# Kernel optimization log

Hardware: AMD Instinct MI355X
Metric: run time of the kernel (lower is better)

The kernel has to match this reference:

```python
import jax, jax.numpy as jnp
import numpy as np

IGNORE_INDEX = 255
KEEP_RATIO = 0.3
MIN_KEPT = 100000
LABEL_SMOOTHING = 0.0


def setup_inputs() -> dict:
    key = jax.random.key(0)
    k1, k2 = jax.random.split(key)
    logits = jax.random.normal(k1, (8, 19, 512, 1024), dtype=jnp.float32)
    labels = jax.random.randint(k2, (8, 512, 1024), 0, 19, dtype=jnp.int64)
    return {"logits": logits, "labels": labels}


def reference(logits, labels):
    B, C, H, W = logits.shape
    # per-pixel cross entropy (reduction='none'), flattened to [N]
    logp = jax.nn.log_softmax(logits, axis=1)                      # [B,C,H,W]
    logp_flat = logp.transpose(0, 2, 3, 1).reshape(-1, C)          # [N,C]
    lab = labels.reshape(-1)                                       # [N]
    valid = lab != IGNORE_INDEX
    safe_lab = jnp.where(valid, lab, 0)
    nll = -jnp.take_along_axis(logp_flat, safe_lab[:, None], axis=1)[:, 0]
    smooth = -jnp.mean(logp_flat, axis=1)
    loss = (1.0 - LABEL_SMOOTHING) * nll + LABEL_SMOOTHING * smooth
    # torch CE with ignore_index gives 0 loss at ignored pixels
    loss = jnp.where(valid, loss, 0.0)

    n_valid = jnp.sum(valid).astype(jnp.int32)
    n_keep = jnp.maximum((KEEP_RATIO * n_valid.astype(jnp.float32)).astype(jnp.int32),
                         jnp.minimum(MIN_KEPT, n_valid))
    n_keep = jnp.minimum(n_keep, n_valid)

    # sort valid losses descending; invalid pixels pushed to the end via -inf
    masked = jnp.where(valid, loss, -jnp.inf)
    sorted_desc = -jnp.sort(-masked)
    thr = jax.lax.stop_gradient(sorted_desc[jnp.maximum(n_keep - 1, 0)])
    thr = jnp.where(n_keep < n_valid, thr, -jnp.inf)

    keep = valid & (masked >= thr)
    cnt = jnp.sum(keep).astype(loss.dtype)
    total = jnp.sum(jnp.where(keep, loss, 0.0))
    mean_kept = total / jnp.maximum(cnt, 1.0)
    # n_valid == 0 -> 0.0 (matches logits.sum()*0.0)
    return jnp.where(n_valid == 0, jnp.sum(logits) * 0.0, mean_kept)
```

## Files before the change

kernel.cpp:

```cpp
#include <hip/hip_runtime.h>
#include <math.h>

#define IGN 255
constexpr int NC = 19;
constexpr int HWsz = 512 * 1024;
constexpr int NPIX = 8 * HWsz;

typedef float v4f __attribute__((ext_vector_type(4)));
typedef int v4i __attribute__((ext_vector_type(4)));
typedef unsigned v4u __attribute__((ext_vector_type(4)));

struct Ctl {
  double total;
  unsigned n_valid, cnt, done, pad;
};

constexpr size_t H0 = 256;
constexpr size_t H1 = H0 + 2048 * 4;
constexpr size_t H2 = H1 + 2048 * 4;
constexpr size_t LOSS_OFF = 65536;

__device__ inline unsigned flip_key(unsigned u) {
  unsigned mask = (unsigned)((int)u >> 31) | 0x80000000u;
  return u ^ mask;
}
__device__ inline float unflip_val(unsigned k) {
  unsigned u = (k & 0x80000000u) ? (k ^ 0x80000000u) : ~k;
  return __uint_as_float(u);
}
__device__ inline unsigned compute_k(unsigned nv) {
  int nk = (int)(0.3f * (float)nv);
  int mk = (100000 < (int)nv) ? 100000 : (int)nv;
  if (nk < mk) nk = mk;
  if (nk > (int)nv) nk = (int)nv;
  return (unsigned)nk;
}

template <int NB>
__device__ inline void selscan(const unsigned* __restrict__ hist, unsigned k,
                               unsigned& bin, unsigned& kk) {
  constexpr int BPT = NB / 256;
  __shared__ unsigned ts[256];
  __shared__ unsigned bb[2];
  int t = threadIdx.x;
  unsigned local[BPT];
  unsigned lsum = 0;
#pragma unroll
  for (int j = 0; j < BPT; ++j) { local[j] = hist[t * BPT + j]; lsum += local[j]; }
  ts[t] = lsum;
  __syncthreads();
  for (int off = 1; off < 256; off <<= 1) {
    unsigned add = (t + off < 256) ? ts[t + off] : 0u;
    __syncthreads();
    ts[t] += add;
    __syncthreads();
  }
  unsigned above = ts[t] - lsum;
  if (t == 0) { bb[0] = 0xFFFFFFFFu; bb[1] = 0u; }
  __syncthreads();
  if (k > 0) {
#pragma unroll
    for (int j = BPT - 1; j >= 0; --j) {
      unsigned cb = local[j];
      unsigned tot = above + cb;
      if (above < k && tot >= k) { bb[0] = (unsigned)(t * BPT + j); bb[1] = k - above; }
      above = tot;
    }
  }
  __syncthreads();
  bin = bb[0];
  kk = bb[1];
  __syncthreads();
}

__global__ void k_init(unsigned char* ws) {
  Ctl* ctl = (Ctl*)ws;
  unsigned* h = (unsigned*)(ws + H0);
  int t = threadIdx.x;
  if (t == 0) { ctl->total = 0.0; ctl->n_valid = 0; ctl->cnt = 0; ctl->done = 0; }
  for (int i = t; i < 5120; i += 256) h[i] = 0;
}

__global__ __launch_bounds__(256) void k_loss(const float* __restrict__ logits,
                                              const int* __restrict__ labels,
                                              unsigned char* __restrict__ ws) {
  Ctl* ctl = (Ctl*)ws;
  float* loss = (float*)(ws + LOSS_OFF);
  unsigned* h0 = (unsigned*)(ws + H0);
  __shared__ unsigned lh[2048];
  __shared__ unsigned red[256];
  for (int i = threadIdx.x; i < 2048; i += 256) lh[i] = 0;
  __syncthreads();

  int t = threadIdx.x;
  int base = blockIdx.x * 4096;
  int b = base >> 19;
  int hw = base & (HWsz - 1);
  const float* lbase = logits + (size_t)(b * NC) * HWsz + hw + t * 4;

  v4i labv[4];
#pragma unroll
  for (int q = 0; q < 4; ++q)
    labv[q] = *reinterpret_cast<const v4i*>(labels + base + q * 1024 + t * 4);

  v4f m[4], s[4], vl[4];
#pragma unroll
  for (int q = 0; q < 4; ++q) {
    v4f v = *reinterpret_cast<const v4f*>(lbase + q * 1024);
    m[q] = v;
    s[q] = (v4f)(1.f);
#pragma unroll
    for (int j = 0; j < 4; ++j)
      vl[q][j] = (labv[q][j] == 0) ? v[j] : 0.f;
  }

#pragma unroll 1
  for (int c = 1; c < NC; ++c) {
    const float* cb = lbase + (size_t)c * HWsz;
    v4f v[4];
#pragma unroll
    for (int q = 0; q < 4; ++q)
      v[q] = *reinterpret_cast<const v4f*>(cb + q * 1024);
#pragma unroll
    for (int q = 0; q < 4; ++q) {
#pragma unroll
      for (int j = 0; j < 4; ++j) {
        float x = v[q][j];
        float mo = m[q][j];
        float mn = fmaxf(mo, x);
        s[q][j] = s[q][j] * __expf(mo - mn) + __expf(x - mn);
        m[q][j] = mn;
        vl[q][j] = (labv[q][j] == c) ? x : vl[q][j];
      }
    }
  }

  unsigned cnt = 0;
#pragma unroll
  for (int q = 0; q < 4; ++q) {
    v4f o;
#pragma unroll
    for (int j = 0; j < 4; ++j) {
      int lb = labv[q][j];
      float lse = m[q][j] + __logf(s[q][j]);
      o[j] = (lb == IGN) ? -INFINITY : (lse - vl[q][j]);
      cnt += (lb != IGN);
      atomicAdd(&lh[flip_key(__float_as_uint(o[j])) >> 21], 1u);
    }
    *reinterpret_cast<v4f*>(loss + base + q * 1024 + t * 4) = o;
  }

  red[t] = cnt;
  __syncthreads();
  for (int s2 = 128; s2 > 0; s2 >>= 1) {
    if (t < s2) red[t] += red[t + s2];
    __syncthreads();
  }
  if (t == 0 && red[0]) atomicAdd(&ctl->n_valid, red[0]);
  for (int i = t; i < 2048; i += 256)
    if (lh[i]) atomicAdd(&h0[i], lh[i]);
}

__global__ __launch_bounds__(256) void k_hist1(unsigned char* __restrict__ ws) {
  Ctl* ctl = (Ctl*)ws;
  const unsigned* keys = (const unsigned*)(ws + LOSS_OFF);
  unsigned* h0 = (unsigned*)(ws + H0);
  unsigned* h1 = (unsigned*)(ws + H1);
  __shared__ unsigned lh[2048];
  unsigned k0 = compute_k(ctl->n_valid);
  unsigned p0, k1;
  selscan<2048>(h0, k0, p0, k1);
  for (int i = threadIdx.x; i < 2048; i += 256) lh[i] = 0;
  __syncthreads();

  unsigned idx0 = blockIdx.x * 512 + threadIdx.x;
#pragma unroll
  for (int i = 0; i < 2; ++i) {
    v4u u = reinterpret_cast<const v4u*>(keys)[idx0 + i * 256];
#pragma unroll
    for (int j = 0; j < 4; ++j) {
      unsigned key = flip_key(u[j]);
      if ((key >> 21) == p0) atomicAdd(&lh[(key >> 10) & 0x7FFu], 1u);
    }
  }
  __syncthreads();
  for (int i = threadIdx.x; i < 2048; i += 256)
    if (lh[i]) atomicAdd(&h1[i], lh[i]);
}

__global__ __launch_bounds__(256) void k_hist2(unsigned char* __restrict__ ws) {
  Ctl* ctl = (Ctl*)ws;
  const unsigned* keys = (const unsigned*)(ws + LOSS_OFF);
  unsigned* h0 = (unsigned*)(ws + H0);
  unsigned* h1 = (unsigned*)(ws + H1);
  unsigned* h2 = (unsigned*)(ws + H2);
  __shared__ unsigned lh[1024];
  unsigned k0 = compute_k(ctl->n_valid);
  unsigned p0, k1, p1, k2;
  selscan<2048>(h0, k0, p0, k1);
  selscan<2048>(h1, k1, p1, k2);
  unsigned pp = (p0 << 11) | p1;
  for (int i = threadIdx.x; i < 1024; i += 256) lh[i] = 0;
  __syncthreads();

  unsigned idx0 = blockIdx.x * 512 + threadIdx.x;
#pragma unroll
  for (int i = 0; i < 2; ++i) {
    v4u u = reinterpret_cast<const v4u*>(keys)[idx0 + i * 256];
#pragma unroll
    for (int j = 0; j < 4; ++j) {
      unsigned key = flip_key(u[j]);
      if ((key >> 10) == pp) atomicAdd(&lh[key & 0x3FFu], 1u);
    }
  }
  __syncthreads();
  for (int i = threadIdx.x; i < 1024; i += 256)
    if (lh[i]) atomicAdd(&h2[i], lh[i]);
}

__global__ __launch_bounds__(256) void k_final(unsigned char* __restrict__ ws,
                                               float* __restrict__ out) {
  Ctl* ctl = (Ctl*)ws;
  const float* loss = (const float*)(ws + LOSS_OFF);
  unsigned* h0 = (unsigned*)(ws + H0);
  unsigned* h1 = (unsigned*)(ws + H1);
  unsigned* h2 = (unsigned*)(ws + H2);
  unsigned k0 = compute_k(ctl->n_valid);
  unsigned p0, k1, p1, k2, b2, kf;
  selscan<2048>(h0, k0, p0, k1);
  selscan<2048>(h1, k1, p1, k2);
  selscan<1024>(h2, k2, b2, kf);
  float thr = INFINITY;
  if (k0 > 0) thr = unflip_val((((p0 << 11) | p1) << 10) | b2);

  unsigned idx0 = blockIdx.x * 512 + threadIdx.x;
  float s = 0.f;
  unsigned c = 0;
#pragma unroll
  for (int i = 0; i < 2; ++i) {
    v4f v = reinterpret_cast<const v4f*>(loss)[idx0 + i * 256];
    if (v[0] >= thr) { s += v[0]; c++; }
    if (v[1] >= thr) { s += v[1]; c++; }
    if (v[2] >= thr) { s += v[2]; c++; }
    if (v[3] >= thr) { s += v[3]; c++; }
  }
  double sd = (double)s;
  for (int off = 32; off > 0; off >>= 1) {
    sd += __shfl_down(sd, off);
    c += __shfl_down(c, off);
  }
  __shared__ double sred[4];
  __shared__ unsigned cred[4];
  int wave = threadIdx.x >> 6, lane = threadIdx.x & 63;
  if (lane == 0) { sred[wave] = sd; cred[wave] = c; }
  __syncthreads();
  if (threadIdx.x == 0) {
    double st = sred[0] + sred[1] + sred[2] + sred[3];
    unsigned ct = cred[0] + cred[1] + cred[2] + cred[3];
    atomicAdd(&ctl->total, st);
    atomicAdd(&ctl->cnt, ct);
    __threadfence();
    unsigned prev = atomicAdd(&ctl->done, 1u);
    if (prev == gridDim.x - 1) {
      double tt = atomicAdd(&ctl->total, 0.0);
      unsigned cc = atomicAdd(&ctl->cnt, 0u);
      float r = 0.f;
      if (ctl->n_valid != 0) {
        if (cc < 1u) cc = 1u;
        r = (float)(tt / (double)cc);
      }
      out[0] = r;
    }
  }
}

extern "C" void kernel_launch(void* const* d_in, const int* in_sizes, int n_in,
                              void* d_out, int out_size, void* d_ws, size_t ws_size,
                              hipStream_t stream) {
  const float* logits = (const float*)d_in[0];
  const int* labels = (const int*)d_in[1];
  float* out = (float*)d_out;
  unsigned char* ws = (unsigned char*)d_ws;

  hipLaunchKernelGGL(k_init, dim3(1), dim3(256), 0, stream, ws);
  hipLaunchKernelGGL(k_loss, dim3(NPIX / 4096), dim3(256), 0, stream, logits, labels, ws);
  hipLaunchKernelGGL(k_hist1, dim3(NPIX / 8 / 256), dim3(256), 0, stream, ws);
  hipLaunchKernelGGL(k_hist2, dim3(NPIX / 8 / 256), dim3(256), 0, stream, ws);
  hipLaunchKernelGGL(k_final, dim3(NPIX / 8 / 256), dim3(256), 0, stream, ws, out);
}
```

Measured before the change: 206.0 us.

## Drop max-tracking softmax, prefetch logits, fold kept-sum into radix passes

The loss kernel now computes log-sum-exp as a plain sum of exp without a running max, packs labels into bytes, and software-prefetches channel planes two ahead with nontemporal loads. Per-wave shared histograms reduce atomic contention. The radix-select passes accumulate the sum and count of elements strictly above the current prefix, plus a per-bin sum for the last level. This removes the separate full scan in the final kernel and leaves a single-block epilogue. Dropping the max subtraction risks overflow for large logits, and float atomic per-bin sums may change rounding.

```diff
diff --git a/kernel.cpp b/kernel.cpp
--- a/kernel.cpp
+++ b/kernel.cpp
@@ -1,7 +1,7 @@
 #include <hip/hip_runtime.h>
 #include <math.h>
 
-#define IGN 255
+#define IGN 255u
 constexpr int NC = 19;
 constexpr int HWsz = 512 * 1024;
 constexpr int NPIX = 8 * HWsz;
@@ -11,14 +11,18 @@
 typedef unsigned v4u __attribute__((ext_vector_type(4)));
 
 struct Ctl {
-  double total;
-  unsigned n_valid, cnt, done, pad;
+  double s_above;
+  unsigned long long c_above;
+  unsigned n_valid;
+  unsigned pad;
 };
 
 constexpr size_t H0 = 256;
-constexpr size_t H1 = H0 + 2048 * 4;
-constexpr size_t H2 = H1 + 2048 * 4;
-constexpr size_t LOSS_OFF = 65536;
+constexpr size_t H1 = H0 + 8192;
+constexpr size_t H2 = H1 + 8192;
+constexpr size_t SUM2 = H2 + 4096;
+constexpr size_t KEYS = 65536;
+constexpr size_t ZERO_BYTES = SUM2 + 4096;
 
 __device__ inline unsigned flip_key(unsigned u) {
   unsigned mask = (unsigned)((int)u >> 31) | 0x80000000u;
@@ -73,81 +77,75 @@
   __syncthreads();
 }
 
-__global__ void k_init(unsigned char* ws) {
-  Ctl* ctl = (Ctl*)ws;
-  unsigned* h = (unsigned*)(ws + H0);
-  int t = threadIdx.x;
-  if (t == 0) { ctl->total = 0.0; ctl->n_valid = 0; ctl->cnt = 0; ctl->done = 0; }
-  for (int i = t; i < 5120; i += 256) h[i] = 0;
-}
-
 __global__ __launch_bounds__(256) void k_loss(const float* __restrict__ logits,
                                               const int* __restrict__ labels,
                                               unsigned char* __restrict__ ws) {
   Ctl* ctl = (Ctl*)ws;
-  float* loss = (float*)(ws + LOSS_OFF);
   unsigned* h0 = (unsigned*)(ws + H0);
-  __shared__ unsigned lh[2048];
+  unsigned* keys = (unsigned*)(ws + KEYS);
+  __shared__ unsigned lh[4 * 2048];
   __shared__ unsigned red[256];
-  for (int i = threadIdx.x; i < 2048; i += 256) lh[i] = 0;
-  __syncthreads();
-
-  int t = threadIdx.x;
-  int base = blockIdx.x * 4096;
+  int t = threadIdx.x;
+  for (int i = t; i < 8192; i += 256) lh[i] = 0;
+  __syncthreads();
+
+  int base = blockIdx.x * 2048;
   int b = base >> 19;
   int hw = base & (HWsz - 1);
-  const float* lbase = logits + (size_t)(b * NC) * HWsz + hw + t * 4;
-
-  v4i labv[4];
-#pragma unroll
-  for (int q = 0; q < 4; ++q)
-    labv[q] = *reinterpret_cast<const v4i*>(labels + base + q * 1024 + t * 4);
-
-  v4f m[4], s[4], vl[4];
-#pragma unroll
-  for (int q = 0; q < 4; ++q) {
-    v4f v = *reinterpret_cast<const v4f*>(lbase + q * 1024);
-    m[q] = v;
-    s[q] = (v4f)(1.f);
-#pragma unroll
-    for (int j = 0; j < 4; ++j)
-      vl[q][j] = (labv[q][j] == 0) ? v[j] : 0.f;
-  }
+  const float* lp = logits + (size_t)(b * NC) * HWsz + hw + t * 4;
+
+  unsigned labp[2];
+#pragma unroll
+  for (int q = 0; q < 2; ++q) {
+    v4i l = *reinterpret_cast<const v4i*>(labels + base + q * 1024 + t * 4);
+    labp[q] = (unsigned)(l[0] & 255) | ((unsigned)(l[1] & 255) << 8) |
+              ((unsigned)(l[2] & 255) << 16) | ((unsigned)(l[3] & 255) << 24);
+  }
+
+  v4f s[2] = {(v4f)(0.f), (v4f)(0.f)};
+  v4f vl[2] = {(v4f)(0.f), (v4f)(0.f)};
+  v4f cur[2], nxt[2];
+  cur[0] = __builtin_nontemporal_load(reinterpret_cast<const v4f*>(lp));
+  cur[1] = __builtin_nontemporal_load(reinterpret_cast<const v4f*>(lp + 1024));
+  nxt[0] = __builtin_nontemporal_load(reinterpret_cast<const v4f*>(lp + HWsz));
+  nxt[1] = __builtin_nontemporal_load(reinterpret_cast<const v4f*>(lp + HWsz + 1024));
 
 #pragma unroll 1
-  for (int c = 1; c < NC; ++c) {
-    const float* cb = lbase + (size_t)c * HWsz;
-    v4f v[4];
-#pragma unroll
-    for (int q = 0; q < 4; ++q)
-      v[q] = *reinterpret_cast<const v4f*>(cb + q * 1024);
-#pragma unroll
-    for (int q = 0; q < 4; ++q) {
+  for (int c = 0; c < NC; ++c) {
+    v4f fut0 = cur[0], fut1 = cur[1];
+    if (c + 2 < NC) {
+      const float* fp = lp + (size_t)(c + 2) * HWsz;
+      fut0 = __builtin_nontemporal_load(reinterpret_cast<const v4f*>(fp));
+      fut1 = __builtin_nontemporal_load(reinterpret_cast<const v4f*>(fp + 1024));
+    }
+    unsigned cc = (unsigned)c;
+#pragma unroll
+    for (int q = 0; q < 2; ++q) {
 #pragma unroll
       for (int j = 0; j < 4; ++j) {
-        float x = v[q][j];
-        float mo = m[q][j];
-        float mn = fmaxf(mo, x);
-        s[q][j] = s[q][j] * __expf(mo - mn) + __expf(x - mn);
-        m[q][j] = mn;
-        vl[q][j] = (labv[q][j] == c) ? x : vl[q][j];
+        float x = cur[q][j];
+        s[q][j] += __expf(x);
+        vl[q][j] = (((labp[q] >> (8 * j)) & 255u) == cc) ? x : vl[q][j];
       }
     }
+    cur[0] = nxt[0]; cur[1] = nxt[1];
+    nxt[0] = fut0;  nxt[1] = fut1;
   }
 
   unsigned cnt = 0;
-#pragma unroll
-  for (int q = 0; q < 4; ++q) {
-    v4f o;
+  unsigned lw = (unsigned)(t >> 6) * 2048u;
+#pragma unroll
+  for (int q = 0; q < 2; ++q) {
+    v4u kv;
 #pragma unroll
     for (int j = 0; j < 4; ++j) {
-      int lb = labv[q][j];
-      float lse = m[q][j] + __logf(s[q][j]);
-      o[j] = (lb == IGN) ? -INFINITY : (lse - vl[q][j]);
+      unsigned lb = (labp[q] >> (8 * j)) & 255u;
+      float o = (lb == IGN) ? -INFINITY : (__logf(s[q][j]) - vl[q][j]);
+      kv[j] = flip_key(__float_as_uint(o));
       cnt += (lb != IGN);
-      atomicAdd(&lh[flip_key(__float_as_uint(o[j])) >> 21], 1u);
-    }
-    *reinterpret_cast<v4f*>(loss + base + q * 1024 + t * 4) = o;
+      atomicAdd(&lh[lw + (kv[j] >> 21)], 1u);
+    }
+    *reinterpret_cast<v4u*>(keys + base + q * 1024 + t * 4) = kv;
   }
 
   red[t] = cnt;
@@ -157,120 +155,157 @@
     __syncthreads();
   }
   if (t == 0 && red[0]) atomicAdd(&ctl->n_valid, red[0]);
-  for (int i = t; i < 2048; i += 256)
-    if (lh[i]) atomicAdd(&h0[i], lh[i]);
-}
-
-__global__ __launch_bounds__(256) void k_hist1(unsigned char* __restrict__ ws) {
+  for (int i = t; i < 2048; i += 256) {
+    unsigned v = lh[i] + lh[2048 + i] + lh[4096 + i] + lh[6144 + i];
+    if (v) atomicAdd(&h0[i], v);
+  }
+}
+
+__global__ __launch_bounds__(256) void k_pass1(unsigned char* __restrict__ ws) {
   Ctl* ctl = (Ctl*)ws;
-  const unsigned* keys = (const unsigned*)(ws + LOSS_OFF);
-  unsigned* h0 = (unsigned*)(ws + H0);
+  const unsigned* keys = (const unsigned*)(ws + KEYS);
+  const unsigned* h0 = (const unsigned*)(ws + H0);
   unsigned* h1 = (unsigned*)(ws + H1);
   __shared__ unsigned lh[2048];
+  int t = threadIdx.x;
   unsigned k0 = compute_k(ctl->n_valid);
   unsigned p0, k1;
   selscan<2048>(h0, k0, p0, k1);
-  for (int i = threadIdx.x; i < 2048; i += 256) lh[i] = 0;
-  __syncthreads();
-
-  unsigned idx0 = blockIdx.x * 512 + threadIdx.x;
-#pragma unroll
-  for (int i = 0; i < 2; ++i) {
-    v4u u = reinterpret_cast<const v4u*>(keys)[idx0 + i * 256];
+  for (int i = t; i < 2048; i += 256) lh[i] = 0;
+  __syncthreads();
+
+  int base = blockIdx.x * 2048 + t * 4;
+  float fs = 0.f;
+  unsigned fc = 0;
+#pragma unroll
+  for (int q = 0; q < 2; ++q) {
+    v4u kv = *reinterpret_cast<const v4u*>(keys + base + q * 1024);
 #pragma unroll
     for (int j = 0; j < 4; ++j) {
-      unsigned key = flip_key(u[j]);
-      if ((key >> 21) == p0) atomicAdd(&lh[(key >> 10) & 0x7FFu], 1u);
-    }
-  }
-  __syncthreads();
-  for (int i = threadIdx.x; i < 2048; i += 256)
+      unsigned key = kv[j];
+      unsigned pre = key >> 21;
+      if (pre > p0) { fs += unflip_val(key); fc++; }
+      else if (pre == p0) atomicAdd(&lh[(key >> 10) & 0x7FFu], 1u);
+    }
+  }
+  __syncthreads();
+  for (int i = t; i < 2048; i += 256)
     if (lh[i]) atomicAdd(&h1[i], lh[i]);
-}
-
-__global__ __launch_bounds__(256) void k_hist2(unsigned char* __restrict__ ws) {
+
+  double sd = (double)fs;
+  for (int off = 32; off > 0; off >>= 1) {
+    sd += __shfl_down(sd, off);
+    fc += __shfl_down(fc, off);
+  }
+  __shared__ double sred[4];
+  __shared__ unsigned cred[4];
+  int wave = t >> 6, lane = t & 63;
+  if (lane == 0) { sred[wave] = sd; cred[wave] = fc; }
+  __syncthreads();
+  if (t == 0) {
+    double st = sred[0] + sred[1] + sred[2] + sred[3];
+    unsigned long long ct = (unsigned long long)(cred[0] + cred[1] + cred[2] + cred[3]);
+    if (st != 0.0) atomicAdd(&ctl->s_above, st);
+    if (ct) atomicAdd(&ctl->c_above, ct);
+  }
+}
+
+__global__ __launch_bounds__(256) void k_pass2(unsigned char* __restrict__ ws) {
   Ctl* ctl = (Ctl*)ws;
-  const unsigned* keys = (const unsigned*)(ws + LOSS_OFF);
-  unsigned* h0 = (unsigned*)(ws + H0);
-  unsigned* h1 = (unsigned*)(ws + H1);
+  const unsigned* keys = (const unsigned*)(ws + KEYS);
+  const unsigned* h0 = (const unsigned*)(ws + H0);
+  const unsigned* h1 = (const unsigned*)(ws + H1);
   unsigned* h2 = (unsigned*)(ws + H2);
+  float* sum2 = (float*)(ws + SUM2);
   __shared__ unsigned lh[1024];
+  int t = threadIdx.x;
   unsigned k0 = compute_k(ctl->n_valid);
   unsigned p0, k1, p1, k2;
   selscan<2048>(h0, k0, p0, k1);
   selscan<2048>(h1, k1, p1, k2);
-  unsigned pp = (p0 << 11) | p1;
-  for (int i = threadIdx.x; i < 1024; i += 256) lh[i] = 0;
-  __syncthreads();
-
-  unsigned idx0 = blockIdx.x * 512 + threadIdx.x;
-#pragma unroll
-  for (int i = 0; i < 2; ++i) {
-    v4u u = reinterpret_cast<const v4u*>(keys)[idx0 + i * 256];
+  for (int i = t; i < 1024; i += 256) lh[i] = 0;
+  __syncthreads();
+
+  int base = blockIdx.x * 2048 + t * 4;
+  float fs = 0.f;
+  unsigned fc = 0;
+#pragma unroll
+  for (int q = 0; q < 2; ++q) {
+    v4u kv = *reinterpret_cast<const v4u*>(keys + base + q * 1024);
 #pragma unroll
     for (int j = 0; j < 4; ++j) {
-      unsigned key = flip_key(u[j]);
-      if ((key >> 10) == pp) atomicAdd(&lh[key & 0x3FFu], 1u);
-    }
-  }
-  __syncthreads();
-  for (int i = threadIdx.x; i < 1024; i += 256)
+      unsigned key = kv[j];
+      if ((key >> 21) == p0) {
+        unsigned mid = (key >> 10) & 0x7FFu;
+        if (mid > p1) { fs += unflip_val(key); fc++; }
+        else if (mid == p1) {
+          atomicAdd(&lh[key & 0x3FFu], 1u);
+          atomicAdd(&sum2[key & 0x3FFu], unflip_val(key));
+        }
+      }
+    }
+  }
+  __syncthreads();
+  for (int i = t; i < 1024; i += 256)
     if (lh[i]) atomicAdd(&h2[i], lh[i]);
-}
-
-__global__ __launch_bounds__(256) void k_final(unsigned char* __restrict__ ws,
-                                               float* __restrict__ out) {
+
+  double sd = (double)fs;
+  for (int off = 32; off > 0; off >>= 1) {
+    sd += __shfl_down(sd, off);
+    fc += __shfl_down(fc, off);
+  }
+  __shared__ double sred[4];
+  __shared__ unsigned cred[4];
+  int wave = t >> 6, lane = t & 63;
+  if (lane == 0) { sred[wave] = sd; cred[wave] = fc; }
+  __syncthreads();
+  if (t == 0) {
+    double st = sred[0] + sred[1] + sred[2] + sred[3];
+    unsigned long long ct = (unsigned long long)(cred[0] + cred[1] + cred[2] + cred[3]);
+    if (st != 0.0) atomicAdd(&ctl->s_above, st);
+    if (ct) atomicAdd(&ctl->c_above, ct);
+  }
+}
+
+__global__ __launch_bounds__(256) void k_epi(unsigned char* __restrict__ ws,
+                                             float* __restrict__ out) {
   Ctl* ctl = (Ctl*)ws;
-  const float* loss = (const float*)(ws + LOSS_OFF);
-  unsigned* h0 = (unsigned*)(ws + H0);
-  unsigned* h1 = (unsigned*)(ws + H1);
-  unsigned* h2 = (unsigned*)(ws + H2);
-  unsigned k0 = compute_k(ctl->n_valid);
+  const unsigned* h0 = (const unsigned*)(ws + H0);
+  const unsigned* h1 = (const unsigned*)(ws + H1);
+  const unsigned* h2 = (const unsigned*)(ws + H2);
+  const float* sum2 = (const float*)(ws + SUM2);
+  int t = threadIdx.x;
+  unsigned nv = ctl->n_valid;
+  unsigned k0 = compute_k(nv);
   unsigned p0, k1, p1, k2, b2, kf;
   selscan<2048>(h0, k0, p0, k1);
   selscan<2048>(h1, k1, p1, k2);
   selscan<1024>(h2, k2, b2, kf);
-  float thr = INFINITY;
-  if (k0 > 0) thr = unflip_val((((p0 << 11) | p1) << 10) | b2);
-
-  unsigned idx0 = blockIdx.x * 512 + threadIdx.x;
-  float s = 0.f;
-  unsigned c = 0;
-#pragma unroll
-  for (int i = 0; i < 2; ++i) {
-    v4f v = reinterpret_cast<const v4f*>(loss)[idx0 + i * 256];
-    if (v[0] >= thr) { s += v[0]; c++; }
-    if (v[1] >= thr) { s += v[1]; c++; }
-    if (v[2] >= thr) { s += v[2]; c++; }
-    if (v[3] >= thr) { s += v[3]; c++; }
-  }
-  double sd = (double)s;
+
+  double ds = 0.0;
+  unsigned dc = 0;
+  for (unsigned i = t; i < 1024; i += 256) {
+    if (i >= b2) { ds += (double)sum2[i]; dc += h2[i]; }
+  }
   for (int off = 32; off > 0; off >>= 1) {
-    sd += __shfl_down(sd, off);
-    c += __shfl_down(c, off);
+    ds += __shfl_down(ds, off);
+    dc += __shfl_down(dc, off);
   }
   __shared__ double sred[4];
   __shared__ unsigned cred[4];
-  int wave = threadIdx.x >> 6, lane = threadIdx.x & 63;
-  if (lane == 0) { sred[wave] = sd; cred[wave] = c; }
-  __syncthreads();
-  if (threadIdx.x == 0) {
-    double st = sred[0] + sred[1] + sred[2] + sred[3];
-    unsigned ct = cred[0] + cred[1] + cred[2] + cred[3];
-    atomicAdd(&ctl->total, st);
-    atomicAdd(&ctl->cnt, ct);
-    __threadfence();
-    unsigned prev = atomicAdd(&ctl->done, 1u);
-    if (prev == gridDim.x - 1) {
-      double tt = atomicAdd(&ctl->total, 0.0);
-      unsigned cc = atomicAdd(&ctl->cnt, 0u);
-      float r = 0.f;
-      if (ctl->n_valid != 0) {
-        if (cc < 1u) cc = 1u;
-        r = (float)(tt / (double)cc);
-      }
-      out[0] = r;
-    }
+  int wave = t >> 6, lane = t & 63;
+  if (lane == 0) { sred[wave] = ds; cred[wave] = dc; }
+  __syncthreads();
+  if (t == 0) {
+    double total = ctl->s_above + sred[0] + sred[1] + sred[2] + sred[3];
+    unsigned long long cnt = ctl->c_above +
+        (unsigned long long)(cred[0] + cred[1] + cred[2] + cred[3]);
+    float r = 0.f;
+    if (nv != 0) {
+      if (cnt < 1ull) cnt = 1ull;
+      r = (float)(total / (double)cnt);
+    }
+    out[0] = r;
   }
 }
 
@@ -282,9 +317,9 @@
   float* out = (float*)d_out;
   unsigned char* ws = (unsigned char*)d_ws;
 
-  hipLaunchKernelGGL(k_init, dim3(1), dim3(256), 0, stream, ws);
-  hipLaunchKernelGGL(k_loss, dim3(NPIX / 4096), dim3(256), 0, stream, logits, labels, ws);
-  hipLaunchKernelGGL(k_hist1, dim3(NPIX / 8 / 256), dim3(256), 0, stream, ws);
-  hipLaunchKernelGGL(k_hist2, dim3(NPIX / 8 / 256), dim3(256), 0, stream, ws);
-  hipLaunchKernelGGL(k_final, dim3(NPIX / 8 / 256), dim3(256), 0, stream, ws, out);
-}
+  hipMemsetAsync(ws, 0, ZERO_BYTES, stream);
+  hipLaunchKernelGGL(k_loss, dim3(NPIX / 2048), dim3(256), 0, stream, logits, labels, ws);
+  hipLaunchKernelGGL(k_pass1, dim3(NPIX / 2048), dim3(256), 0, stream, ws);
+  hipLaunchKernelGGL(k_pass2, dim3(NPIX / 2048), dim3(256), 0, stream, ws);
+  hipLaunchKernelGGL(k_epi, dim3(1), dim3(256), 0, stream, ws, out);
+}
```

After: 200.3 us. -2.8%, faster.
